# Kernel tuning notes

Measured on AMD Instinct MI355X. Metric: run time of the kernel, lower is better.

Reference implementation:

```python
import jax, jax.numpy as jnp
import numpy as np

N = 50000      # nodes
E = 800000     # edges (avg degree 16)
IN, H, OUT = 128, 128, 64


def setup_inputs() -> dict:
    key = jax.random.key(0)
    k1, k2, k3, k4 = jax.random.split(key, 4)
    x = jax.random.normal(k1, (N, IN), dtype=jnp.float32)
    edge_index = jax.random.randint(k2, (2, E), 0, N, dtype=jnp.int32)
    W1 = jax.random.normal(k3, (IN, H), dtype=jnp.float32) * (1.0 / np.sqrt(IN))
    b1 = jnp.zeros((H,), dtype=jnp.float32)
    W2 = jax.random.normal(k4, (H, OUT), dtype=jnp.float32) * (1.0 / np.sqrt(H))
    b2 = jnp.zeros((OUT,), dtype=jnp.float32)
    return {"x": x, "edge_index": edge_index, "W1": W1, "b1": b1, "W2": W2, "b2": b2}


def gcn_conv(x, edge_index, W, b):
    """PyG GCNConv: D^-1/2 (A + I) D^-1/2 (x W) + b, with self-loops."""
    src, dst = edge_index[0], edge_index[1]
    h = x @ W                                              # [N, F_out] transform first (F_out <= F_in path)
    ones = jnp.ones((src.shape[0],), dtype=h.dtype)
    deg = jax.ops.segment_sum(ones, dst, num_segments=N) + 1.0  # +1 for self-loop
    inv_sqrt_deg = jax.lax.rsqrt(deg)
    norm = inv_sqrt_deg[src] * inv_sqrt_deg[dst]           # [E]
    agg = jax.ops.segment_sum(h[src] * norm[:, None], dst, num_segments=N)
    # self-loop contribution: norm_ii = deg_i^-1
    return agg + h * (1.0 / deg)[:, None] + b


def reference(x, edge_index, W1, b1, W2, b2):
    h = jax.nn.relu(gcn_conv(x, edge_index, W1, b1))
    return gcn_conv(h, edge_index, W2, b2)
```

## Files before the change

### kernel.cpp

```cpp
#include <hip/hip_runtime.h>
#include <hip/hip_bf16.h>


#define GCN_IN   128
#define GCN_H    128
#define GCN_OUT  64
#define CAP      64
#define OVF_CAP  65536
#define SCAT_BLOCKS 1024

__device__ __forceinline__ ushort f2bf(float f) {
    uint b = __float_as_uint(f);
    b = (b + 0x7FFFu + ((b >> 16) & 1u)) >> 16;
    return (ushort)b;
}
__device__ __forceinline__ float bf2f_lo(uint u) { return __uint_as_float(u << 16); }
__device__ __forceinline__ float bf2f_hi(uint u) { return __uint_as_float(u & 0xFFFF0000u); }

__global__ __launch_bounds__(256) void k_fused1(
        const int* __restrict__ src, const int* __restrict__ dst,
        int* __restrict__ cnt, int* __restrict__ slot,
        int* __restrict__ ovfcnt, int2* __restrict__ ovf, int E,
        const float* __restrict__ A, const float* __restrict__ B,
        ushort* __restrict__ C, int M, int N) {
    __shared__ float At[32][68];
    __shared__ float Bs[32][64];
    const int tid = threadIdx.x;

    if (blockIdx.x < SCAT_BLOCKS) {
        const int part = blockIdx.x & 7;
        const int psz  = (N + 7) >> 3;
        const int lo   = part * psz;
        const int hi   = min(lo + psz, N);
        const int bip  = blockIdx.x >> 3;
        const int stride = (SCAT_BLOCKS >> 3) * 256;
        for (int e = bip * 256 + tid; e < E; e += stride) {
            int d = __builtin_nontemporal_load(dst + e);
            int s = __builtin_nontemporal_load(src + e);
            if (d >= lo && d < hi) {
                int pos = atomicAdd(&cnt[d], 1);
                if (pos < CAP) {
                    slot[(size_t)d * CAP + pos] = s;
                } else {
                    int q = atomicAdd(ovfcnt, 1);
                    if (q < OVF_CAP) ovf[q] = make_int2(d, s);
                }
            }
        }
        return;
    }

    const int g = blockIdx.x - SCAT_BLOCKS;
    const int row0 = (g >> 1) * 64;
    const int col0 = (g & 1) * 64;
    const int tx = tid & 15;
    const int ty = tid >> 4;
    float acc[4][4] = {};

    for (int kb = 0; kb < 128; kb += 32) {
        #pragma unroll
        for (int t = 0; t < 2; ++t) {
            int f = tid * 4 + t * 1024;
            int r = f >> 5;
            int k = f & 31;
            float4 v = make_float4(0.f, 0.f, 0.f, 0.f);
            int gr = row0 + r;
            if (gr < M) v = *(const float4*)(A + (size_t)gr * 128 + kb + k);
            At[k + 0][r] = v.x;
            At[k + 1][r] = v.y;
            At[k + 2][r] = v.z;
            At[k + 3][r] = v.w;
        }
        #pragma unroll
        for (int t = 0; t < 2; ++t) {
            int f = tid * 4 + t * 1024;
            int r = f >> 6;
            int c = f & 63;
            *(float4*)&Bs[r][c] = *(const float4*)(B + (size_t)(kb + r) * 128 + col0 + c);
        }
        __syncthreads();
        #pragma unroll 8
        for (int k = 0; k < 32; ++k) {
            float4 a = *(const float4*)&At[k][ty * 4];
            float4 b = *(const float4*)&Bs[k][tx * 4];
            acc[0][0] += a.x * b.x; acc[0][1] += a.x * b.y; acc[0][2] += a.x * b.z; acc[0][3] += a.x * b.w;
            acc[1][0] += a.y * b.x; acc[1][1] += a.y * b.y; acc[1][2] += a.y * b.z; acc[1][3] += a.y * b.w;
            acc[2][0] += a.z * b.x; acc[2][1] += a.z * b.y; acc[2][2] += a.z * b.z; acc[2][3] += a.z * b.w;
            acc[3][0] += a.w * b.x; acc[3][1] += a.w * b.y; acc[3][2] += a.w * b.z; acc[3][3] += a.w * b.w;
        }
        __syncthreads();
    }
    #pragma unroll
    for (int i = 0; i < 4; ++i) {
        int gr = row0 + ty * 4 + i;
        if (gr < M) {
            ushort4 o;
            o.x = f2bf(acc[i][0]); o.y = f2bf(acc[i][1]);
            o.z = f2bf(acc[i][2]); o.w = f2bf(acc[i][3]);
            *(ushort4*)(C + (size_t)gr * 128 + col0 + tx * 4) = o;
        }
    }
}

__global__ __launch_bounds__(256) void k_gemm2(const ushort* __restrict__ A,
                                               const float* __restrict__ B,
                                               ushort* __restrict__ C, int M) {
    __shared__ float At[32][68];
    __shared__ float Bs[32][64];
    const int tid = threadIdx.x;
    const int row0 = blockIdx.x * 64;
    const int tx = tid & 15;
    const int ty = tid >> 4;
    float acc[4][4] = {};

    for (int kb = 0; kb < 128; kb += 32) {
        #pragma unroll
        for (int t = 0; t < 2; ++t) {
            int f = tid * 4 + t * 1024;
            int r = f >> 5;
            int k = f & 31;
            uint2 v = make_uint2(0u, 0u);
            int gr = row0 + r;
            if (gr < M) v = *(const uint2*)(A + (size_t)gr * 128 + kb + k);
            At[k + 0][r] = bf2f_lo(v.x);
            At[k + 1][r] = bf2f_hi(v.x);
            At[k + 2][r] = bf2f_lo(v.y);
            At[k + 3][r] = bf2f_hi(v.y);
        }
        #pragma unroll
        for (int t = 0; t < 2; ++t) {
            int f = tid * 4 + t * 1024;
            int r = f >> 6;
            int c = f & 63;
            *(float4*)&Bs[r][c] = *(const float4*)(B + (size_t)(kb + r) * 64 + c);
        }
        __syncthreads();
        #pragma unroll 8
        for (int k = 0; k < 32; ++k) {
            float4 a = *(const float4*)&At[k][ty * 4];
            float4 b = *(const float4*)&Bs[k][tx * 4];
            acc[0][0] += a.x * b.x; acc[0][1] += a.x * b.y; acc[0][2] += a.x * b.z; acc[0][3] += a.x * b.w;
            acc[1][0] += a.y * b.x; acc[1][1] += a.y * b.y; acc[1][2] += a.y * b.z; acc[1][3] += a.y * b.w;
            acc[2][0] += a.z * b.x; acc[2][1] += a.z * b.y; acc[2][2] += a.z * b.z; acc[2][3] += a.z * b.w;
            acc[3][0] += a.w * b.x; acc[3][1] += a.w * b.y; acc[3][2] += a.w * b.z; acc[3][3] += a.w * b.w;
        }
        __syncthreads();
    }
    #pragma unroll
    for (int i = 0; i < 4; ++i) {
        int gr = row0 + ty * 4 + i;
        if (gr < M) {
            ushort4 o;
            o.x = f2bf(acc[i][0]); o.y = f2bf(acc[i][1]);
            o.z = f2bf(acc[i][2]); o.w = f2bf(acc[i][3]);
            *(ushort4*)(C + (size_t)gr * 64 + tx * 4) = o;
        }
    }
}

__global__ __launch_bounds__(256) void k_agg128(const ushort* __restrict__ h,
                                                const int* __restrict__ cnt,
                                                const int* __restrict__ slot,
                                                const float* __restrict__ bias,
                                                const int* __restrict__ ovfcnt,
                                                const int2* __restrict__ ovf,
                                                ushort* __restrict__ out, int n) {
    int node = (blockIdx.x * 256 + threadIdx.x) >> 6;
    int lane = threadIdx.x & 63;
    if (node >= n) return;
    int deg = cnt[node];
    int degm = min(deg, CAP);
    float isd_i = rsqrtf((float)(deg + 1));
    int idx = slot[(size_t)node * CAP + lane];
    bool valid = lane < degm;
    int sidx = valid ? idx : 0;
    float wl = valid ? rsqrtf((float)(cnt[sidx] + 1)) : 0.f;

    const int q = lane >> 4;
    const int i = lane & 15;
    const ushort* hp = h + 8 * i;

    float acc[8] = {};
    for (int j = 0; j < degm; j += 8) {
        int j0 = j + q;
        int j1 = j + 4 + q;
        int   s0 = __shfl(sidx, j0);
        int   s1 = __shfl(sidx, j1);
        float w0 = __shfl(wl, j0);
        float w1 = __shfl(wl, j1);
        uint4 v0 = *(const uint4*)(hp + (size_t)s0 * 128);
        uint4 v1 = *(const uint4*)(hp + (size_t)s1 * 128);
        acc[0] += w0 * bf2f_lo(v0.x) + w1 * bf2f_lo(v1.x);
        acc[1] += w0 * bf2f_hi(v0.x) + w1 * bf2f_hi(v1.x);
        acc[2] += w0 * bf2f_lo(v0.y) + w1 * bf2f_lo(v1.y);
        acc[3] += w0 * bf2f_hi(v0.y) + w1 * bf2f_hi(v1.y);
        acc[4] += w0 * bf2f_lo(v0.z) + w1 * bf2f_lo(v1.z);
        acc[5] += w0 * bf2f_hi(v0.z) + w1 * bf2f_hi(v1.z);
        acc[6] += w0 * bf2f_lo(v0.w) + w1 * bf2f_lo(v1.w);
        acc[7] += w0 * bf2f_hi(v0.w) + w1 * bf2f_hi(v1.w);
    }
    int ovn = *ovfcnt;
    for (int t = 0; t < ovn; ++t) {
        int2 p = ovf[t];
        if (p.x == node && q == 0) {
            float w0 = rsqrtf((float)(cnt[p.y] + 1));
            uint4 v0 = *(const uint4*)(hp + (size_t)p.y * 128);
            acc[0] += w0 * bf2f_lo(v0.x); acc[1] += w0 * bf2f_hi(v0.x);
            acc[2] += w0 * bf2f_lo(v0.y); acc[3] += w0 * bf2f_hi(v0.y);
            acc[4] += w0 * bf2f_lo(v0.z); acc[5] += w0 * bf2f_hi(v0.z);
            acc[6] += w0 * bf2f_lo(v0.w); acc[7] += w0 * bf2f_hi(v0.w);
        }
    }
    #pragma unroll
    for (int k = 0; k < 8; ++k) {
        acc[k] += __shfl_xor(acc[k], 16);
        acc[k] += __shfl_xor(acc[k], 32);
    }
    if (q == 0) {
        uint4 vs = *(const uint4*)(hp + (size_t)node * 128);
        float4 ba = *(const float4*)(bias + 8 * i);
        float4 bb = *(const float4*)(bias + 8 * i + 4);
        float r0 = fmaxf((acc[0] + isd_i * bf2f_lo(vs.x)) * isd_i + ba.x, 0.f);
        float r1 = fmaxf((acc[1] + isd_i * bf2f_hi(vs.x)) * isd_i + ba.y, 0.f);
        float r2 = fmaxf((acc[2] + isd_i * bf2f_lo(vs.y)) * isd_i + ba.z, 0.f);
        float r3 = fmaxf((acc[3] + isd_i * bf2f_hi(vs.y)) * isd_i + ba.w, 0.f);
        float r4 = fmaxf((acc[4] + isd_i * bf2f_lo(vs.z)) * isd_i + bb.x, 0.f);
        float r5 = fmaxf((acc[5] + isd_i * bf2f_hi(vs.z)) * isd_i + bb.y, 0.f);
        float r6 = fmaxf((acc[6] + isd_i * bf2f_lo(vs.w)) * isd_i + bb.z, 0.f);
        float r7 = fmaxf((acc[7] + isd_i * bf2f_hi(vs.w)) * isd_i + bb.w, 0.f);
        uint4 o;
        o.x = (uint)f2bf(r0) | ((uint)f2bf(r1) << 16);
        o.y = (uint)f2bf(r2) | ((uint)f2bf(r3) << 16);
        o.z = (uint)f2bf(r4) | ((uint)f2bf(r5) << 16);
        o.w = (uint)f2bf(r6) | ((uint)f2bf(r7) << 16);
        *(uint4*)(out + (size_t)node * 128 + 8 * i) = o;
    }
}

__global__ __launch_bounds__(256) void k_agg64(const ushort* __restrict__ h,
                                               const int* __restrict__ cnt,
                                               const int* __restrict__ slot,
                                               const float* __restrict__ bias,
                                               const int* __restrict__ ovfcnt,
                                               const int2* __restrict__ ovf,
                                               float* __restrict__ out, int n) {
    int node = (blockIdx.x * 256 + threadIdx.x) >> 6;
    int lane = threadIdx.x & 63;
    if (node >= n) return;
    int deg = cnt[node];
    int degm = min(deg, CAP);
    float isd_i = rsqrtf((float)(deg + 1));
    int idx = slot[(size_t)node * CAP + lane];
    bool valid = lane < degm;
    int sidx = valid ? idx : 0;
    float wl = valid ? rsqrtf((float)(cnt[sidx] + 1)) : 0.f;

    const int g = lane >> 3;
    const int i = lane & 7;
    const ushort* hp = h + 8 * i;

    float acc[8] = {};
    for (int j = 0; j < degm; j += 16) {
        int j0 = j + g;
        int j1 = j + 8 + g;
        int   s0 = __shfl(sidx, j0);
        int   s1 = __shfl(sidx, j1);
        float w0 = __shfl(wl, j0);
        float w1 = __shfl(wl, j1);
        uint4 v0 = *(const uint4*)(hp + (size_t)s0 * 64);
        uint4 v1 = *(const uint4*)(hp + (size_t)s1 * 64);
        acc[0] += w0 * bf2f_lo(v0.x) + w1 * bf2f_lo(v1.x);
        acc[1] += w0 * bf2f_hi(v0.x) + w1 * bf2f_hi(v1.x);
        acc[2] += w0 * bf2f_lo(v0.y) + w1 * bf2f_lo(v1.y);
        acc[3] += w0 * bf2f_hi(v0.y) + w1 * bf2f_hi(v1.y);
        acc[4] += w0 * bf2f_lo(v0.z) + w1 * bf2f_lo(v1.z);
        acc[5] += w0 * bf2f_hi(v0.z) + w1 * bf2f_hi(v1.z);
        acc[6] += w0 * bf2f_lo(v0.w) + w1 * bf2f_lo(v1.w);
        acc[7] += w0 * bf2f_hi(v0.w) + w1 * bf2f_hi(v1.w);
    }
    int ovn = *ovfcnt;
    for (int t = 0; t < ovn; ++t) {
        int2 p = ovf[t];
        if (p.x == node && g == 0) {
            float w0 = rsqrtf((float)(cnt[p.y] + 1));
            uint4 v0 = *(const uint4*)(hp + (size_t)p.y * 64);
            acc[0] += w0 * bf2f_lo(v0.x); acc[1] += w0 * bf2f_hi(v0.x);
            acc[2] += w0 * bf2f_lo(v0.y); acc[3] += w0 * bf2f_hi(v0.y);
            acc[4] += w0 * bf2f_lo(v0.z); acc[5] += w0 * bf2f_hi(v0.z);
            acc[6] += w0 * bf2f_lo(v0.w); acc[7] += w0 * bf2f_hi(v0.w);
        }
    }
    #pragma unroll
    for (int k = 0; k < 8; ++k) {
        acc[k] += __shfl_xor(acc[k], 8);
        acc[k] += __shfl_xor(acc[k], 16);
        acc[k] += __shfl_xor(acc[k], 32);
    }
    if (g == 0) {
        uint4 vs = *(const uint4*)(hp + (size_t)node * 64);
        float4 ba = *(const float4*)(bias + 8 * i);
        float4 bb = *(const float4*)(bias + 8 * i + 4);
        float4 r0, r1;
        r0.x = (acc[0] + isd_i * bf2f_lo(vs.x)) * isd_i + ba.x;
        r0.y = (acc[1] + isd_i * bf2f_hi(vs.x)) * isd_i + ba.y;
        r0.z = (acc[2] + isd_i * bf2f_lo(vs.y)) * isd_i + ba.z;
        r0.w = (acc[3] + isd_i * bf2f_hi(vs.y)) * isd_i + ba.w;
        r1.x = (acc[4] + isd_i * bf2f_lo(vs.z)) * isd_i + bb.x;
        r1.y = (acc[5] + isd_i * bf2f_hi(vs.z)) * isd_i + bb.y;
        r1.z = (acc[6] + isd_i * bf2f_lo(vs.w)) * isd_i + bb.z;
        r1.w = (acc[7] + isd_i * bf2f_hi(vs.w)) * isd_i + bb.w;
        float* op = out + (size_t)node * 64 + 8 * i;
        *(float4*)op = r0;
        *(float4*)(op + 4) = r1;
    }
}

static inline size_t align256(size_t x) { return (x + 255) & ~(size_t)255; }

extern "C" void kernel_launch(void* const* d_in, const int* in_sizes, int n_in,
                              void* d_out, int out_size, void* d_ws, size_t ws_size,
                              hipStream_t stream) {
    const float* x  = (const float*)d_in[0];
    const int*   ei = (const int*)d_in[1];
    const float* W1 = (const float*)d_in[2];
    const float* b1 = (const float*)d_in[3];
    const float* W2 = (const float*)d_in[4];
    const float* b2 = (const float*)d_in[5];
    float* out = (float*)d_out;

    const int N = in_sizes[0] / GCN_IN;
    const int E = in_sizes[1] / 2;
    const int* src = ei;
    const int* dst = ei + E;

    char* ws = (char*)d_ws;
    size_t o = 0;
    int*    cnt    = (int*)(ws + o);     o += align256((size_t)N * 4);
    int*    ovfcnt = (int*)(ws + o);     o += 256;
    int2*   ovf    = (int2*)(ws + o);    o += align256((size_t)OVF_CAP * 8);
    int*    slot   = (int*)(ws + o);     o += align256((size_t)N * CAP * 4);
    ushort* hb     = (ushort*)(ws + o);  o += align256((size_t)N * GCN_H * 2);
    ushort* h1b    = (ushort*)(ws + o);  o += align256((size_t)N * GCN_H * 2);
    ushort* h2b    = (ushort*)(ws + o);  o += align256((size_t)N * GCN_OUT * 2);

    hipMemsetAsync(cnt, 0, align256((size_t)N * 4) + 256, stream);

    {
        int gemm_blocks = ((N + 63) / 64) * 2;
        k_fused1<<<SCAT_BLOCKS + gemm_blocks, 256, 0, stream>>>(
            src, dst, cnt, slot, ovfcnt, ovf, E, x, W1, hb, N, N);
    }

    k_agg128<<<(N * 64 + 255) / 256, 256, 0, stream>>>(hb, cnt, slot, b1,
                                                       ovfcnt, ovf, h1b, N);
    k_gemm2<<<(N + 63) / 64, 256, 0, stream>>>(h1b, W2, h2b, N);

    k_agg64<<<(N * 64 + 255) / 256, 256, 0, stream>>>(h2b, cnt, slot, b2,
                                                      ovfcnt, ovf, out, N);
}
```

Measured before the change: 213.7 us.

## Pre-scale GEMM outputs by source inverse-sqrt degree and store neighbor slots as ushort

The source-side normalization rsqrt(deg+1) now multiplies each row in the GEMM epilogue, so the aggregation kernels no longer gather cnt for every neighbor and only apply a validity mask. Neighbor slots become 16-bit, which halves slot traffic. This relies on node indices fitting in 16 bits, and N=50000 does. Scatter and GEMM1 are split into separate kernels because GEMM1 now needs the final degree counts, which gives up the overlap the fused kernel had.

```diff
diff --git a/kernel.cpp b/kernel.cpp
--- a/kernel.cpp
+++ b/kernel.cpp
@@ -17,42 +17,40 @@
 __device__ __forceinline__ float bf2f_lo(uint u) { return __uint_as_float(u << 16); }
 __device__ __forceinline__ float bf2f_hi(uint u) { return __uint_as_float(u & 0xFFFF0000u); }
 
-__global__ __launch_bounds__(256) void k_fused1(
+__global__ __launch_bounds__(256) void k_scatter(
         const int* __restrict__ src, const int* __restrict__ dst,
-        int* __restrict__ cnt, int* __restrict__ slot,
-        int* __restrict__ ovfcnt, int2* __restrict__ ovf, int E,
-        const float* __restrict__ A, const float* __restrict__ B,
-        ushort* __restrict__ C, int M, int N) {
+        int* __restrict__ cnt, ushort* __restrict__ slot,
+        int* __restrict__ ovfcnt, int2* __restrict__ ovf, int E, int N) {
+    const int part = blockIdx.x & 7;
+    const int psz  = (N + 7) >> 3;
+    const int lo   = part * psz;
+    const int hi   = min(lo + psz, N);
+    const int bip  = blockIdx.x >> 3;
+    const int stride = (SCAT_BLOCKS >> 3) * 256;
+    for (int e = bip * 256 + threadIdx.x; e < E; e += stride) {
+        int d = __builtin_nontemporal_load(dst + e);
+        int s = __builtin_nontemporal_load(src + e);
+        if (d >= lo && d < hi) {
+            int pos = atomicAdd(&cnt[d], 1);
+            if (pos < CAP) {
+                slot[(size_t)d * CAP + pos] = (ushort)s;
+            } else {
+                int q = atomicAdd(ovfcnt, 1);
+                if (q < OVF_CAP) ovf[q] = make_int2(d, s);
+            }
+        }
+    }
+}
+
+__global__ __launch_bounds__(256) void k_gemm1(const float* __restrict__ A,
+                                               const float* __restrict__ B,
+                                               const int* __restrict__ cnt,
+                                               ushort* __restrict__ C, int M) {
     __shared__ float At[32][68];
     __shared__ float Bs[32][64];
     const int tid = threadIdx.x;
-
-    if (blockIdx.x < SCAT_BLOCKS) {
-        const int part = blockIdx.x & 7;
-        const int psz  = (N + 7) >> 3;
-        const int lo   = part * psz;
-        const int hi   = min(lo + psz, N);
-        const int bip  = blockIdx.x >> 3;
-        const int stride = (SCAT_BLOCKS >> 3) * 256;
-        for (int e = bip * 256 + tid; e < E; e += stride) {
-            int d = __builtin_nontemporal_load(dst + e);
-            int s = __builtin_nontemporal_load(src + e);
-            if (d >= lo && d < hi) {
-                int pos = atomicAdd(&cnt[d], 1);
-                if (pos < CAP) {
-                    slot[(size_t)d * CAP + pos] = s;
-                } else {
-                    int q = atomicAdd(ovfcnt, 1);
-                    if (q < OVF_CAP) ovf[q] = make_int2(d, s);
-                }
-            }
-        }
-        return;
-    }
-
-    const int g = blockIdx.x - SCAT_BLOCKS;
-    const int row0 = (g >> 1) * 64;
-    const int col0 = (g & 1) * 64;
+    const int row0 = blockIdx.x * 64;
+    const int col0 = blockIdx.y * 64;
     const int tx = tid & 15;
     const int ty = tid >> 4;
     float acc[4][4] = {};
@@ -94,9 +92,10 @@
     for (int i = 0; i < 4; ++i) {
         int gr = row0 + ty * 4 + i;
         if (gr < M) {
+            float w = rsqrtf((float)(cnt[gr] + 1));
             ushort4 o;
-            o.x = f2bf(acc[i][0]); o.y = f2bf(acc[i][1]);
-            o.z = f2bf(acc[i][2]); o.w = f2bf(acc[i][3]);
+            o.x = f2bf(w * acc[i][0]); o.y = f2bf(w * acc[i][1]);
+            o.z = f2bf(w * acc[i][2]); o.w = f2bf(w * acc[i][3]);
             *(ushort4*)(C + (size_t)gr * 128 + col0 + tx * 4) = o;
         }
     }
@@ -104,6 +103,7 @@
 
 __global__ __launch_bounds__(256) void k_gemm2(const ushort* __restrict__ A,
                                                const float* __restrict__ B,
+                                               const int* __restrict__ cnt,
                                                ushort* __restrict__ C, int M) {
     __shared__ float At[32][68];
     __shared__ float Bs[32][64];
@@ -150,9 +150,10 @@
     for (int i = 0; i < 4; ++i) {
         int gr = row0 + ty * 4 + i;
         if (gr < M) {
+            float w = rsqrtf((float)(cnt[gr] + 1));
             ushort4 o;
-            o.x = f2bf(acc[i][0]); o.y = f2bf(acc[i][1]);
-            o.z = f2bf(acc[i][2]); o.w = f2bf(acc[i][3]);
+            o.x = f2bf(w * acc[i][0]); o.y = f2bf(w * acc[i][1]);
+            o.z = f2bf(w * acc[i][2]); o.w = f2bf(w * acc[i][3]);
             *(ushort4*)(C + (size_t)gr * 64 + tx * 4) = o;
         }
     }
@@ -160,7 +161,7 @@
 
 __global__ __launch_bounds__(256) void k_agg128(const ushort* __restrict__ h,
                                                 const int* __restrict__ cnt,
-                                                const int* __restrict__ slot,
+                                                const ushort* __restrict__ slot,
                                                 const float* __restrict__ bias,
                                                 const int* __restrict__ ovfcnt,
                                                 const int2* __restrict__ ovf,
@@ -171,10 +172,7 @@
     int deg = cnt[node];
     int degm = min(deg, CAP);
     float isd_i = rsqrtf((float)(deg + 1));
-    int idx = slot[(size_t)node * CAP + lane];
-    bool valid = lane < degm;
-    int sidx = valid ? idx : 0;
-    float wl = valid ? rsqrtf((float)(cnt[sidx] + 1)) : 0.f;
+    int sidx = (int)__builtin_nontemporal_load(slot + (size_t)node * CAP + lane);
 
     const int q = lane >> 4;
     const int i = lane & 15;
@@ -186,8 +184,8 @@
         int j1 = j + 4 + q;
         int   s0 = __shfl(sidx, j0);
         int   s1 = __shfl(sidx, j1);
-        float w0 = __shfl(wl, j0);
-        float w1 = __shfl(wl, j1);
+        float w0 = (j0 < degm) ? 1.f : 0.f;
+        float w1 = (j1 < degm) ? 1.f : 0.f;
         uint4 v0 = *(const uint4*)(hp + (size_t)s0 * 128);
         uint4 v1 = *(const uint4*)(hp + (size_t)s1 * 128);
         acc[0] += w0 * bf2f_lo(v0.x) + w1 * bf2f_lo(v1.x);
@@ -203,12 +201,11 @@
     for (int t = 0; t < ovn; ++t) {
         int2 p = ovf[t];
         if (p.x == node && q == 0) {
-            float w0 = rsqrtf((float)(cnt[p.y] + 1));
             uint4 v0 = *(const uint4*)(hp + (size_t)p.y * 128);
-            acc[0] += w0 * bf2f_lo(v0.x); acc[1] += w0 * bf2f_hi(v0.x);
-            acc[2] += w0 * bf2f_lo(v0.y); acc[3] += w0 * bf2f_hi(v0.y);
-            acc[4] += w0 * bf2f_lo(v0.z); acc[5] += w0 * bf2f_hi(v0.z);
-            acc[6] += w0 * bf2f_lo(v0.w); acc[7] += w0 * bf2f_hi(v0.w);
+            acc[0] += bf2f_lo(v0.x); acc[1] += bf2f_hi(v0.x);
+            acc[2] += bf2f_lo(v0.y); acc[3] += bf2f_hi(v0.y);
+            acc[4] += bf2f_lo(v0.z); acc[5] += bf2f_hi(v0.z);
+            acc[6] += bf2f_lo(v0.w); acc[7] += bf2f_hi(v0.w);
         }
     }
     #pragma unroll
@@ -220,14 +217,14 @@
         uint4 vs = *(const uint4*)(hp + (size_t)node * 128);
         float4 ba = *(const float4*)(bias + 8 * i);
         float4 bb = *(const float4*)(bias + 8 * i + 4);
-        float r0 = fmaxf((acc[0] + isd_i * bf2f_lo(vs.x)) * isd_i + ba.x, 0.f);
-        float r1 = fmaxf((acc[1] + isd_i * bf2f_hi(vs.x)) * isd_i + ba.y, 0.f);
-        float r2 = fmaxf((acc[2] + isd_i * bf2f_lo(vs.y)) * isd_i + ba.z, 0.f);
-        float r3 = fmaxf((acc[3] + isd_i * bf2f_hi(vs.y)) * isd_i + ba.w, 0.f);
-        float r4 = fmaxf((acc[4] + isd_i * bf2f_lo(vs.z)) * isd_i + bb.x, 0.f);
-        float r5 = fmaxf((acc[5] + isd_i * bf2f_hi(vs.z)) * isd_i + bb.y, 0.f);
-        float r6 = fmaxf((acc[6] + isd_i * bf2f_lo(vs.w)) * isd_i + bb.z, 0.f);
-        float r7 = fmaxf((acc[7] + isd_i * bf2f_hi(vs.w)) * isd_i + bb.w, 0.f);
+        float r0 = fmaxf((acc[0] + bf2f_lo(vs.x)) * isd_i + ba.x, 0.f);
+        float r1 = fmaxf((acc[1] + bf2f_hi(vs.x)) * isd_i + ba.y, 0.f);
+        float r2 = fmaxf((acc[2] + bf2f_lo(vs.y)) * isd_i + ba.z, 0.f);
+        float r3 = fmaxf((acc[3] + bf2f_hi(vs.y)) * isd_i + ba.w, 0.f);
+        float r4 = fmaxf((acc[4] + bf2f_lo(vs.z)) * isd_i + bb.x, 0.f);
+        float r5 = fmaxf((acc[5] + bf2f_hi(vs.z)) * isd_i + bb.y, 0.f);
+        float r6 = fmaxf((acc[6] + bf2f_lo(vs.w)) * isd_i + bb.z, 0.f);
+        float r7 = fmaxf((acc[7] + bf2f_hi(vs.w)) * isd_i + bb.w, 0.f);
         uint4 o;
         o.x = (uint)f2bf(r0) | ((uint)f2bf(r1) << 16);
         o.y = (uint)f2bf(r2) | ((uint)f2bf(r3) << 16);
@@ -239,7 +236,7 @@
 
 __global__ __launch_bounds__(256) void k_agg64(const ushort* __restrict__ h,
                                                const int* __restrict__ cnt,
-                                               const int* __restrict__ slot,
+                                               const ushort* __restrict__ slot,
                                                const float* __restrict__ bias,
                                                const int* __restrict__ ovfcnt,
                                                const int2* __restrict__ ovf,
@@ -250,10 +247,7 @@
     int deg = cnt[node];
     int degm = min(deg, CAP);
     float isd_i = rsqrtf((float)(deg + 1));
-    int idx = slot[(size_t)node * CAP + lane];
-    bool valid = lane < degm;
-    int sidx = valid ? idx : 0;
-    float wl = valid ? rsqrtf((float)(cnt[sidx] + 1)) : 0.f;
+    int sidx = (int)__builtin_nontemporal_load(slot + (size_t)node * CAP + lane);
 
     const int g = lane >> 3;
     const int i = lane & 7;
@@ -265,8 +259,8 @@
         int j1 = j + 8 + g;
         int   s0 = __shfl(sidx, j0);
         int   s1 = __shfl(sidx, j1);
-        float w0 = __shfl(wl, j0);
-        float w1 = __shfl(wl, j1);
+        float w0 = (j0 < degm) ? 1.f : 0.f;
+        float w1 = (j1 < degm) ? 1.f : 0.f;
         uint4 v0 = *(const uint4*)(hp + (size_t)s0 * 64);
         uint4 v1 = *(const uint4*)(hp + (size_t)s1 * 64);
         acc[0] += w0 * bf2f_lo(v0.x) + w1 * bf2f_lo(v1.x);
@@ -282,12 +276,11 @@
     for (int t = 0; t < ovn; ++t) {
         int2 p = ovf[t];
         if (p.x == node && g == 0) {
-            float w0 = rsqrtf((float)(cnt[p.y] + 1));
             uint4 v0 = *(const uint4*)(hp + (size_t)p.y * 64);
-            acc[0] += w0 * bf2f_lo(v0.x); acc[1] += w0 * bf2f_hi(v0.x);
-            acc[2] += w0 * bf2f_lo(v0.y); acc[3] += w0 * bf2f_hi(v0.y);
-            acc[4] += w0 * bf2f_lo(v0.z); acc[5] += w0 * bf2f_hi(v0.z);
-            acc[6] += w0 * bf2f_lo(v0.w); acc[7] += w0 * bf2f_hi(v0.w);
+            acc[0] += bf2f_lo(v0.x); acc[1] += bf2f_hi(v0.x);
+            acc[2] += bf2f_lo(v0.y); acc[3] += bf2f_hi(v0.y);
+            acc[4] += bf2f_lo(v0.z); acc[5] += bf2f_hi(v0.z);
+            acc[6] += bf2f_lo(v0.w); acc[7] += bf2f_hi(v0.w);
         }
     }
     #pragma unroll
@@ -301,14 +294,14 @@
         float4 ba = *(const float4*)(bias + 8 * i);
         float4 bb = *(const float4*)(bias + 8 * i + 4);
         float4 r0, r1;
-        r0.x = (acc[0] + isd_i * bf2f_lo(vs.x)) * isd_i + ba.x;
-        r0.y = (acc[1] + isd_i * bf2f_hi(vs.x)) * isd_i + ba.y;
-        r0.z = (acc[2] + isd_i * bf2f_lo(vs.y)) * isd_i + ba.z;
-        r0.w = (acc[3] + isd_i * bf2f_hi(vs.y)) * isd_i + ba.w;
-        r1.x = (acc[4] + isd_i * bf2f_lo(vs.z)) * isd_i + bb.x;
-        r1.y = (acc[5] + isd_i * bf2f_hi(vs.z)) * isd_i + bb.y;
-        r1.z = (acc[6] + isd_i * bf2f_lo(vs.w)) * isd_i + bb.z;
-        r1.w = (acc[7] + isd_i * bf2f_hi(vs.w)) * isd_i + bb.w;
+        r0.x = (acc[0] + bf2f_lo(vs.x)) * isd_i + ba.x;
+        r0.y = (acc[1] + bf2f_hi(vs.x)) * isd_i + ba.y;
+        r0.z = (acc[2] + bf2f_lo(vs.y)) * isd_i + ba.z;
+        r0.w = (acc[3] + bf2f_hi(vs.y)) * isd_i + ba.w;
+        r1.x = (acc[4] + bf2f_lo(vs.z)) * isd_i + bb.x;
+        r1.y = (acc[5] + bf2f_hi(vs.z)) * isd_i + bb.y;
+        r1.z = (acc[6] + bf2f_lo(vs.w)) * isd_i + bb.z;
+        r1.w = (acc[7] + bf2f_hi(vs.w)) * isd_i + bb.w;
         float* op = out + (size_t)node * 64 + 8 * i;
         *(float4*)op = r0;
         *(float4*)(op + 4) = r1;
@@ -338,22 +331,24 @@
     int*    cnt    = (int*)(ws + o);     o += align256((size_t)N * 4);
     int*    ovfcnt = (int*)(ws + o);     o += 256;
     int2*   ovf    = (int2*)(ws + o);    o += align256((size_t)OVF_CAP * 8);
-    int*    slot   = (int*)(ws + o);     o += align256((size_t)N * CAP * 4);
+    ushort* slot   = (ushort*)(ws + o);  o += align256((size_t)N * CAP * 2);
     ushort* hb     = (ushort*)(ws + o);  o += align256((size_t)N * GCN_H * 2);
     ushort* h1b    = (ushort*)(ws + o);  o += align256((size_t)N * GCN_H * 2);
     ushort* h2b    = (ushort*)(ws + o);  o += align256((size_t)N * GCN_OUT * 2);
 
     hipMemsetAsync(cnt, 0, align256((size_t)N * 4) + 256, stream);
 
+    k_scatter<<<SCAT_BLOCKS, 256, 0, stream>>>(src, dst, cnt, slot,
+                                               ovfcnt, ovf, E, N);
+
     {
-        int gemm_blocks = ((N + 63) / 64) * 2;
-        k_fused1<<<SCAT_BLOCKS + gemm_blocks, 256, 0, stream>>>(
-            src, dst, cnt, slot, ovfcnt, ovf, E, x, W1, hb, N, N);
+        dim3 g((N + 63) / 64, 2);
+        k_gemm1<<<g, 256, 0, stream>>>(x, W1, cnt, hb, N);
     }
 
     k_agg128<<<(N * 64 + 255) / 256, 256, 0, stream>>>(hb, cnt, slot, b1,
                                                        ovfcnt, ovf, h1b, N);
-    k_gemm2<<<(N + 63) / 64, 256, 0, stream>>>(h1b, W2, h2b, N);
+    k_gemm2<<<(N + 63) / 64, 256, 0, stream>>>(h1b, W2, cnt, h2b, N);
 
     k_agg64<<<(N * 64 + 255) / 256, 256, 0, stream>>>(h2b, cnt, slot, b2,
                                                       ovfcnt, ovf, out, N);
```

New measurement: 218.9 us. 1.02x slower.
